# Performance work log

Hardware: AMD Instinct MI355X
Metric: run time of the kernel (lower is better)

## Reference

```python
import jax, jax.numpy as jnp
import numpy as np
from jax import lax

T, A, F = 32, 32, 4          # tokens, analyses per token, feats per analysis
E = 256; FE = F * E          # feat emb dim, flattened analysis emb (1024)
H = 768; H2 = 2 * H          # encoder hidden (bi), decoder hidden 1536
DTOK = 256; DDEC = FE + DTOK # decoder input: analysis emb + token emb
V = 50000; VTOK = 30000


def setup_inputs() -> dict:
    key = jax.random.key(0)
    ks = jax.random.split(key, 16)
    g = lambda k, sh, s=0.02: (jax.random.normal(k, sh, jnp.float32) * s)
    return {
        "lattice": jax.random.randint(ks[0], (1, T, A, F), 0, V),
        "lattice_mask": jnp.ones((1, T, A), bool),
        "inputs": jax.random.randint(ks[1], (1, T), 0, VTOK),
        "input_lengths": jnp.full((1, 1, 1), T, jnp.int32),
        "gold_indices": jax.random.randint(ks[2], (1, T), 0, A),
        "sos_ids": jax.random.randint(ks[3], (F,), 0, V),
        "emb_table": g(ks[4], (V, E), 0.1),
        "tok_emb_table": g(ks[5], (VTOK, DTOK), 0.1),
        "enc_Wx_f": g(ks[6], (FE, 4 * H)),
        "enc_Wh_f": g(ks[7], (H, 4 * H)),
        "enc_b_f": jnp.zeros(4 * H, jnp.float32),
        "enc_Wx_b": g(ks[8], (FE, 4 * H)),
        "enc_Wh_b": g(ks[9], (H, 4 * H)),
        "enc_b_b": jnp.zeros(4 * H, jnp.float32),
        "dec_Wx": g(ks[10], (DDEC, 4 * H2)),
        "dec_Wh": g(ks[11], (H2, 4 * H2)),
        "dec_b": jnp.zeros(4 * H2, jnp.float32),
        "attn_W": g(ks[12], (H2, H2)),
    }


def _lstm(xs, Wx, Wh, b, hsize, reverse=False):
    # torch LSTM gate order: i, f, g, o
    def step(carry, x):
        h, c = carry
        gt = x @ Wx + h @ Wh + b
        i, f, g, o = jnp.split(gt, 4)
        c = jax.nn.sigmoid(f) * c + jax.nn.sigmoid(i) * jnp.tanh(g)
        h = jax.nn.sigmoid(o) * jnp.tanh(c)
        return (h, c), h
    init = (jnp.zeros(hsize, xs.dtype), jnp.zeros(hsize, xs.dtype))
    (h, c), ys = lax.scan(step, init, xs, reverse=reverse)
    return ys, h, c


def reference(lattice, lattice_mask, inputs, input_lengths, gold_indices, sos_ids,
              emb_table, tok_emb_table,
              enc_Wx_f, enc_Wh_f, enc_b_f, enc_Wx_b, enc_Wh_b, enc_b_b,
              dec_Wx, dec_Wh, dec_b, attn_W):
    # lattice_emb: per-feat embedding, flattened per analysis -> [1,T,A,FE]
    embed_lattice = emb_table[lattice].reshape(1, T, A, FE)
    # mask is all-True, so mask-packing == flatten: [T*A, FE]
    packed = embed_lattice.reshape(T * A, FE)
    ys_f, hf, cf = _lstm(packed, enc_Wx_f, enc_Wh_f, enc_b_f, H)
    ys_b, hb, cb = _lstm(packed, enc_Wx_b, enc_Wh_b, enc_b_b, H, reverse=True)
    enc = jnp.concatenate([ys_f, ys_b], axis=-1).reshape(T, A, H2)  # per-token slices
    h0 = jnp.concatenate([hf, hb])  # decoder init = concat(fwd,bwd) final states
    c0 = jnp.concatenate([cf, cb])
    tok_emb = tok_emb_table[inputs[0]]          # [T, DTOK]
    sos_emb = emb_table[sos_ids].reshape(FE)    # SOS analysis embedding
    lat = embed_lattice[0]                      # [T, A, FE]

    def step(carry, xs_t):
        h, c, prev = carry
        enc_t, tok_t, g_t, lat_t = xs_t
        x = jnp.concatenate([prev, tok_t])      # [DDEC]
        gt = x @ dec_Wx + h @ dec_Wh + dec_b
        i, f, g, o = jnp.split(gt, 4)
        c_n = jax.nn.sigmoid(f) * c + jax.nn.sigmoid(i) * jnp.tanh(g)
        h_n = jax.nn.sigmoid(o) * jnp.tanh(c_n)
        score = (h_n @ attn_W) @ enc_t.T        # bilinear attention scores [A]
        # teacher forcing: next analysis emb gathered by gold index
        return (h_n, c_n, lat_t[g_t]), score

    _, scores = lax.scan(step, (h0, c0, sos_emb), (enc, tok_emb, gold_indices[0], lat))
    return scores[None]  # [1, T, A]
```

## Files before the change

### kernel.cpp

```cpp
#include <hip/hip_runtime.h>
#include <cstddef>
#include <cstdint>

#define T_ 32
#define A_ 32
#define F_ 4
#define E_ 256
#define FE_ 1024
#define H_ 768
#define H2_ 1536
#define G4_ 3072
#define G8_ 6144
#define DTOK_ 256
#define DDEC_ 1280
#define SEQ_ 1024

constexpr size_t OFF_PACKED  = 0;
constexpr size_t OFF_XF      = OFF_PACKED + 1024ull*1024;
constexpr size_t OFF_XB      = OFF_XF + 1024ull*3072;
constexpr size_t OFF_XD      = OFF_XB + 1024ull*3072;
constexpr size_t OFF_XDIN    = OFF_XD + 32*6144;
constexpr size_t OFF_ENC     = OFF_XDIN + 32*1280;
constexpr size_t OFF_HN      = OFF_ENC + 1024ull*1536;
constexpr size_t OFF_AMAT    = OFF_HN + 32*1536;
constexpr size_t OFF_C0      = OFF_AMAT + 32*1536;
constexpr size_t OFF_PAIRS_E = OFF_C0 + 1536;
constexpr size_t OFF_PAIRS_D = OFF_PAIRS_E + 6144;
constexpr size_t MEMSET_BYTES = (6144 + 6144) * 4;

__device__ __forceinline__ float sigf(float x) { return 1.f / (1.f + __expf(-x)); }

__global__ void embed_k(const int* __restrict__ lattice, const int* __restrict__ inputs,
                        const int* __restrict__ gold, const int* __restrict__ sos,
                        const float* __restrict__ emb, const float* __restrict__ tok_emb,
                        float* __restrict__ packed, float* __restrict__ xdec_in) {
    int b = blockIdx.x, tid = threadIdx.x;
    if (b < SEQ_) {
        #pragma unroll
        for (int f = 0; f < F_; ++f) {
            int vid = lattice[b * F_ + f];
            packed[(size_t)b * FE_ + f * E_ + tid] = emb[(size_t)vid * E_ + tid];
        }
    } else {
        int t = b - SEQ_;
        for (int j = tid; j < DDEC_; j += 256) {
            float v;
            if (j < FE_) {
                int f = j >> 8, e2 = j & 255;
                int vid = (t == 0) ? sos[f]
                                   : lattice[(((t - 1) * A_) + gold[t - 1]) * F_ + f];
                v = emb[(size_t)vid * E_ + e2];
            } else {
                v = tok_emb[(size_t)inputs[t] * DTOK_ + (j - FE_)];
            }
            xdec_in[(size_t)t * DDEC_ + j] = v;
        }
    }
}

#define BM 128
#define BN 128
#define BK 8
__device__ __forceinline__ void gemm_body(
    const float* __restrict__ A, const float* __restrict__ B,
    const float* __restrict__ bias, float* __restrict__ C,
    int M, int N, int K, int n0, int m0, int swh) {
    __shared__ float As[BK][BM + 4];
    __shared__ float Bs[BK][BN + 4];
    int tid = threadIdx.x;
    int tx = tid & 15, ty = tid >> 4;
    int lam = tid >> 1, lak = (tid & 1) * 4;
    int lbk = tid >> 5, lbn = (tid & 31) * 4;
    float acc[8][8] = {};
    for (int k0 = 0; k0 < K; k0 += BK) {
        float4 av = make_float4(0.f, 0.f, 0.f, 0.f);
        if (m0 + lam < M)
            av = *(const float4*)(A + (size_t)(m0 + lam) * K + k0 + lak);
        float4 bv = *(const float4*)(B + (size_t)(k0 + lbk) * N + n0 + lbn);
        __syncthreads();
        As[lak + 0][lam] = av.x; As[lak + 1][lam] = av.y;
        As[lak + 2][lam] = av.z; As[lak + 3][lam] = av.w;
        *(float4*)&Bs[lbk][lbn] = bv;
        __syncthreads();
        #pragma unroll
        for (int kk = 0; kk < BK; ++kk) {
            float a[8], b[8];
            *(float4*)&a[0] = *(const float4*)&As[kk][ty * 8];
            *(float4*)&a[4] = *(const float4*)&As[kk][ty * 8 + 4];
            *(float4*)&b[0] = *(const float4*)&Bs[kk][tx * 8];
            *(float4*)&b[4] = *(const float4*)&Bs[kk][tx * 8 + 4];
            #pragma unroll
            for (int i = 0; i < 8; ++i)
                #pragma unroll
                for (int j = 0; j < 8; ++j)
                    acc[i][j] += a[i] * b[j];
        }
    }
    int qg = 0, jb = 0;
    if (swh) { qg = n0 / swh; jb = n0 - qg * swh; }
    #pragma unroll
    for (int i = 0; i < 8; ++i) {
        int m = m0 + ty * 8 + i;
        if (m >= M) break;
        #pragma unroll
        for (int j = 0; j < 8; ++j) {
            int n = n0 + tx * 8 + j;
            float bb = bias ? bias[n] : 0.f;
            float v = acc[i][j] + bb;
            if (swh) {
                int jc = jb + tx * 8 + j;
                n = (jc / 12) * 48 + (jc % 12) * 4 + qg;
            }
            C[(size_t)m * N + n] = v;
        }
    }
}

__global__ __launch_bounds__(256) void gemm_bias_k(
    const float* __restrict__ A, const float* __restrict__ B,
    const float* __restrict__ bias, float* __restrict__ C,
    int M, int N, int K, int swh) {
    gemm_body(A, B, bias, C, M, N, K, blockIdx.x * BN, blockIdx.y * BM, swh);
}

__global__ __launch_bounds__(256) void gemm_bias2_k(
    const float* __restrict__ A,
    const float* __restrict__ B0, const float* __restrict__ bias0, float* __restrict__ C0,
    const float* __restrict__ B1, const float* __restrict__ bias1, float* __restrict__ C1,
    int M, int N, int K, int swh) {
    const float* B = blockIdx.z ? B1 : B0;
    const float* bias = blockIdx.z ? bias1 : bias0;
    float* C = blockIdx.z ? C1 : C0;
    gemm_body(A, B, bias, C, M, N, K, blockIdx.x * BN, blockIdx.y * BM, swh);
}

__global__ __launch_bounds__(768, 1) void lstm_enc_k(
    const float* __restrict__ Xf, const float* __restrict__ Xb,
    const float* __restrict__ Whf, const float* __restrict__ Whb,
    float* __restrict__ enc, unsigned long long* __restrict__ pairsE,
    unsigned long long* __restrict__ pairsD, float* __restrict__ c0) {
    const int dir = blockIdx.x >> 6;
    const int wb  = blockIdx.x & 63;
    const float* X  = dir ? Xb : Xf;
    const float* Wh = dir ? Whb : Whf;
    unsigned long long* pp = pairsE + (size_t)dir * 1536;
    const int tid = threadIdx.x;
    const int w = tid >> 6, lane = tid & 63;
    const int g16 = lane >> 4;
    const int jg = wb * 12 + w;
    const int d = lane >> 2, q = lane & 3;

    float wgt[3][4][4];
    #pragma unroll
    for (int i = 0; i < 3; ++i)
        #pragma unroll
        for (int e = 0; e < 4; ++e) {
            int k = 4 * lane + e + 256 * i;
            #pragma unroll
            for (int g = 0; g < 4; ++g)
                wgt[i][e][g] = Wh[(size_t)k * G4_ + g * H_ + jg];
        }
    #pragma unroll
    for (int i = 0; i < 3; ++i)
        #pragma unroll
        for (int e = 0; e < 4; ++e)
            #pragma unroll
            for (int g = 0; g < 4; ++g)
                asm volatile("" : "+v"(wgt[i][e][g]));

    __shared__ float h_s[2][768];
    __shared__ float part[4][64];
    float c = 0.f;

    for (int t = 0; t < SEQ_; ++t) {
        const int row = dir ? (SEQ_ - 1 - t) : t;
        float xq = 0.f;
        if (w == 0 && lane < 48) xq = X[(size_t)row * G4_ + wb * 48 + lane];

        const int par = t & 1;
        unsigned long long* p = pp + par * 768 + tid;
        unsigned long long v = __hip_atomic_load(p, __ATOMIC_RELAXED, __HIP_MEMORY_SCOPE_AGENT);
        while ((unsigned)(v >> 32) != (unsigned)t)
            v = __hip_atomic_load(p, __ATOMIC_RELAXED, __HIP_MEMORY_SCOPE_AGENT);
        h_s[par][tid] = __uint_as_float((unsigned)v);
        __syncthreads();

        float a0 = 0.f, a1 = 0.f, a2 = 0.f, a3 = 0.f;
        #pragma unroll
        for (int i = 0; i < 3; ++i) {
            const float4 hv = *(const float4*)&h_s[par][4 * lane + 256 * i];
            a0 += wgt[i][0][0] * hv.x + wgt[i][1][0] * hv.y + wgt[i][2][0] * hv.z + wgt[i][3][0] * hv.w;
            a1 += wgt[i][0][1] * hv.x + wgt[i][1][1] * hv.y + wgt[i][2][1] * hv.z + wgt[i][3][1] * hv.w;
            a2 += wgt[i][0][2] * hv.x + wgt[i][1][2] * hv.y + wgt[i][2][2] * hv.z + wgt[i][3][2] * hv.w;
            a3 += wgt[i][0][3] * hv.x + wgt[i][1][3] * hv.y + wgt[i][2][3] * hv.z + wgt[i][3][3] * hv.w;
        }
        #pragma unroll
        for (int m = 1; m < 16; m <<= 1) {
            a0 += __shfl_xor(a0, m); a1 += __shfl_xor(a1, m);
            a2 += __shfl_xor(a2, m); a3 += __shfl_xor(a3, m);
        }
        if ((lane & 15) == 0)
            *(float4*)&part[g16][w * 4] = make_float4(a0, a1, a2, a3);
        __syncthreads();

        if (w == 0) {
            float s = part[0][lane] + part[1][lane] + part[2][lane] + part[3][lane] + xq;
            float tr = (q == 2) ? tanhf(s) : sigf(s);
            float b1 = __shfl_xor(tr, 1), b2 = __shfl_xor(tr, 2), b3 = __shfl_xor(tr, 3);
            float I  = (q == 0) ? tr : (q == 1) ? b1 : (q == 2) ? b2 : b3;
            float Fv = (q == 0) ? b1 : (q == 1) ? tr : (q == 2) ? b3 : b2;
            float G  = (q == 0) ? b2 : (q == 1) ? b3 : (q == 2) ? tr : b1;
            float O  = (q == 0) ? b3 : (q == 1) ? b2 : (q == 2) ? b1 : tr;
            c = Fv * c + I * G;
            float h = O * tanhf(c);
            float hc = __shfl(h, lane * 4);
            if (lane < 12) {
                enc[(size_t)row * H2_ + dir * H_ + wb * 12 + lane] = hc;
                unsigned long long pk = ((unsigned long long)(unsigned)(t + 1) << 32)
                                      | (unsigned long long)__float_as_uint(hc);
                __hip_atomic_store(pp + ((t + 1) & 1) * 768 + wb * 12 + lane, pk,
                                   __ATOMIC_RELAXED, __HIP_MEMORY_SCOPE_AGENT);
            }
            if (t == SEQ_ - 1) {
                float cc = __shfl(c, lane * 4);
                if (lane < 12) {
                    __hip_atomic_store(pairsD + (size_t)(dir * H_ + wb * 12 + lane),
                                       (unsigned long long)__float_as_uint(hc),
                                       __ATOMIC_RELAXED, __HIP_MEMORY_SCOPE_AGENT);
                    c0[dir * H_ + wb * 12 + lane] = cc;
                }
            }
        }
    }
}

__global__ __launch_bounds__(768, 1) void lstm_dec_k(
    const float* __restrict__ Xd, const float* __restrict__ Wh,
    float* __restrict__ Hn, unsigned long long* __restrict__ pairs,
    const float* __restrict__ c0) {
    const int wb = blockIdx.x;
    const int tid = threadIdx.x;
    const int w = tid >> 6, lane = tid & 63;
    const int g16 = lane >> 4;
    const int jg = wb * 12 + w;
    const int d = lane >> 2, q = lane & 3;

    float wgt[6][4][4];
    #pragma unroll
    for (int i = 0; i < 6; ++i)
        #pragma unroll
        for (int e = 0; e < 4; ++e) {
            int k = 4 * lane + e + 256 * i;
            #pragma unroll
            for (int g = 0; g < 4; ++g)
                wgt[i][e][g] = Wh[(size_t)k * G8_ + g * H2_ + jg];
        }
    #pragma unroll
    for (int i = 0; i < 6; ++i)
        #pragma unroll
        for (int e = 0; e < 4; ++e)
            #pragma unroll
            for (int g = 0; g < 4; ++g)
                asm volatile("" : "+v"(wgt[i][e][g]));

    __shared__ float h_s[2][1536];
    __shared__ float part[4][64];
    float c = (w == 0 && lane < 48) ? c0[wb * 12 + d] : 0.f;

    for (int t = 0; t < T_; ++t) {
        float xq = 0.f;
        if (w == 0 && lane < 48) xq = Xd[(size_t)t * G8_ + wb * 48 + lane];

        const int par = t & 1;
        unsigned long long* p0 = pairs + par * 1536 + tid;
        unsigned long long* p1 = p0 + 768;
        unsigned long long v0 = __hip_atomic_load(p0, __ATOMIC_RELAXED, __HIP_MEMORY_SCOPE_AGENT);
        unsigned long long v1 = __hip_atomic_load(p1, __ATOMIC_RELAXED, __HIP_MEMORY_SCOPE_AGENT);
        while ((unsigned)(v0 >> 32) != (unsigned)t)
            v0 = __hip_atomic_load(p0, __ATOMIC_RELAXED, __HIP_MEMORY_SCOPE_AGENT);
        while ((unsigned)(v1 >> 32) != (unsigned)t)
            v1 = __hip_atomic_load(p1, __ATOMIC_RELAXED, __HIP_MEMORY_SCOPE_AGENT);
        h_s[par][tid]       = __uint_as_float((unsigned)v0);
        h_s[par][tid + 768] = __uint_as_float((unsigned)v1);
        __syncthreads();

        float a0 = 0.f, a1 = 0.f, a2 = 0.f, a3 = 0.f;
        #pragma unroll
        for (int i = 0; i < 6; ++i) {
            const float4 hv = *(const float4*)&h_s[par][4 * lane + 256 * i];
            a0 += wgt[i][0][0] * hv.x + wgt[i][1][0] * hv.y + wgt[i][2][0] * hv.z + wgt[i][3][0] * hv.w;
            a1 += wgt[i][0][1] * hv.x + wgt[i][1][1] * hv.y + wgt[i][2][1] * hv.z + wgt[i][3][1] * hv.w;
            a2 += wgt[i][0][2] * hv.x + wgt[i][1][2] * hv.y + wgt[i][2][2] * hv.z + wgt[i][3][2] * hv.w;
            a3 += wgt[i][0][3] * hv.x + wgt[i][1][3] * hv.y + wgt[i][2][3] * hv.z + wgt[i][3][3] * hv.w;
        }
        #pragma unroll
        for (int m = 1; m < 16; m <<= 1) {
            a0 += __shfl_xor(a0, m); a1 += __shfl_xor(a1, m);
            a2 += __shfl_xor(a2, m); a3 += __shfl_xor(a3, m);
        }
        if ((lane & 15) == 0)
            *(float4*)&part[g16][w * 4] = make_float4(a0, a1, a2, a3);
        __syncthreads();

        if (w == 0) {
            float s = part[0][lane] + part[1][lane] + part[2][lane] + part[3][lane] + xq;
            float tr = (q == 2) ? tanhf(s) : sigf(s);
            float b1 = __shfl_xor(tr, 1), b2 = __shfl_xor(tr, 2), b3 = __shfl_xor(tr, 3);
            float I  = (q == 0) ? tr : (q == 1) ? b1 : (q == 2) ? b2 : b3;
            float Fv = (q == 0) ? b1 : (q == 1) ? tr : (q == 2) ? b3 : b2;
            float G  = (q == 0) ? b2 : (q == 1) ? b3 : (q == 2) ? tr : b1;
            float O  = (q == 0) ? b3 : (q == 1) ? b2 : (q == 2) ? b1 : tr;
            c = Fv * c + I * G;
            float h = O * tanhf(c);
            float hc = __shfl(h, lane * 4);
            if (lane < 12) {
                Hn[(size_t)t * H2_ + wb * 12 + lane] = hc;
                unsigned long long pk = ((unsigned long long)(unsigned)(t + 1) << 32)
                                      | (unsigned long long)__float_as_uint(hc);
                __hip_atomic_store(pairs + ((t + 1) & 1) * 1536 + wb * 12 + lane, pk,
                                   __ATOMIC_RELAXED, __HIP_MEMORY_SCOPE_AGENT);
            }
        }
    }
}

__global__ void score_k(const float* __restrict__ Amat, const float* __restrict__ enc,
                        float* __restrict__ outp) {
    int t = blockIdx.x, tid = threadIdx.x;
    __shared__ float a_s[H2_];
    for (int i = tid; i < H2_; i += 256) a_s[i] = Amat[(size_t)t * H2_ + i];
    __syncthreads();
    int aa = tid >> 3, p = tid & 7;
    const float4* e = (const float4*)(enc + (size_t)(t * A_ + aa) * H2_ + p * 192);
    const float4* ap = (const float4*)(a_s + p * 192);
    float s = 0.f;
    #pragma unroll
    for (int i = 0; i < 48; ++i) {
        float4 av = ap[i], ev = e[i];
        s += av.x * ev.x + av.y * ev.y + av.z * ev.z + av.w * ev.w;
    }
    s += __shfl_xor(s, 1); s += __shfl_xor(s, 2); s += __shfl_xor(s, 4);
    if (p == 0) outp[t * A_ + aa] = s;
}

extern "C" void kernel_launch(void* const* d_in, const int* in_sizes, int n_in,
                              void* d_out, int out_size, void* d_ws, size_t ws_size,
                              hipStream_t stream) {
    const int*   lattice = (const int*)d_in[0];
    const int*   inputs  = (const int*)d_in[2];
    const int*   gold    = (const int*)d_in[4];
    const int*   sos     = (const int*)d_in[5];
    const float* emb     = (const float*)d_in[6];
    const float* tok     = (const float*)d_in[7];
    const float* Wxf = (const float*)d_in[8];
    const float* Whf = (const float*)d_in[9];
    const float* bf  = (const float*)d_in[10];
    const float* Wxb = (const float*)d_in[11];
    const float* Whb = (const float*)d_in[12];
    const float* bb  = (const float*)d_in[13];
    const float* dWx = (const float*)d_in[14];
    const float* dWh = (const float*)d_in[15];
    const float* db  = (const float*)d_in[16];
    const float* aW  = (const float*)d_in[17];
    float* ws  = (float*)d_ws;
    float* out = (float*)d_out;

    float* packed = ws + OFF_PACKED;
    float* Xf     = ws + OFF_XF;
    float* Xb     = ws + OFF_XB;
    float* Xd     = ws + OFF_XD;
    float* xdin   = ws + OFF_XDIN;
    float* enc    = ws + OFF_ENC;
    float* Hn     = ws + OFF_HN;
    float* Amat   = ws + OFF_AMAT;
    float* c0     = ws + OFF_C0;
    unsigned long long* pairsE = (unsigned long long*)(ws + OFF_PAIRS_E);
    unsigned long long* pairsD = (unsigned long long*)(ws + OFF_PAIRS_D);

    hipMemsetAsync((char*)d_ws + OFF_PAIRS_E * sizeof(float), 0, MEMSET_BYTES, stream);

    embed_k<<<SEQ_ + T_, 256, 0, stream>>>(lattice, inputs, gold, sos, emb, tok,
                                           packed, xdin);
    gemm_bias2_k<<<dim3(G4_ / BN, SEQ_ / BM, 2), 256, 0, stream>>>(
        packed, Wxf, bf, Xf, Wxb, bb, Xb, SEQ_, G4_, FE_, H_);
    gemm_bias_k<<<dim3(G8_ / BN, 1), 256, 0, stream>>>(xdin, dWx, db, Xd,
                                                       T_, G8_, DDEC_, H2_);
    lstm_enc_k<<<128, 768, 0, stream>>>(Xf, Xb, Whf, Whb, enc, pairsE, pairsD, c0);
    lstm_dec_k<<<128, 768, 0, stream>>>(Xd, dWh, Hn, pairsD, c0);
    gemm_bias_k<<<dim3(H2_ / BN, 1), 256, 0, stream>>>(Hn, aW, nullptr, Amat,
                                                       T_, H2_, H2_, 0);
    score_k<<<T_, 256, 0, stream>>>(Amat, enc, out);
}
```

Measured before the change: 3.224 ms.

## Halve encoder LSTM block count with two hidden units per warp, add spin sleep

The encoder recurrent kernel now runs 32 blocks per direction instead of 64. Each warp keeps weights for two hidden units in registers, so each block covers 24 units. The goal is fewer blocks taking part in the per-step global atomic handshake, with fewer flag loads and less contention. In exchange each block does twice the arithmetic per step and holds twice the register-resident weights, which risks spilling. The gate-input GEMM's output interleave is made configurable to match the new grouping, and s_sleep is added to the spin-wait loops in both recurrent kernels to cut polling pressure, at the cost of some wake-up latency.

```diff
diff --git a/kernel.cpp b/kernel.cpp
--- a/kernel.cpp
+++ b/kernel.cpp
@@ -64,7 +64,7 @@
 __device__ __forceinline__ void gemm_body(
     const float* __restrict__ A, const float* __restrict__ B,
     const float* __restrict__ bias, float* __restrict__ C,
-    int M, int N, int K, int n0, int m0, int swh) {
+    int M, int N, int K, int n0, int m0, int swh, int dbs) {
     __shared__ float As[BK][BM + 4];
     __shared__ float Bs[BK][BN + 4];
     int tid = threadIdx.x;
@@ -109,7 +109,7 @@
             float v = acc[i][j] + bb;
             if (swh) {
                 int jc = jb + tx * 8 + j;
-                n = (jc / 12) * 48 + (jc % 12) * 4 + qg;
+                n = (jc / dbs) * (4 * dbs) + (jc % dbs) * 4 + qg;
             }
             C[(size_t)m * N + n] = v;
         }
@@ -119,19 +119,19 @@
 __global__ __launch_bounds__(256) void gemm_bias_k(
     const float* __restrict__ A, const float* __restrict__ B,
     const float* __restrict__ bias, float* __restrict__ C,
-    int M, int N, int K, int swh) {
-    gemm_body(A, B, bias, C, M, N, K, blockIdx.x * BN, blockIdx.y * BM, swh);
+    int M, int N, int K, int swh, int dbs) {
+    gemm_body(A, B, bias, C, M, N, K, blockIdx.x * BN, blockIdx.y * BM, swh, dbs);
 }
 
 __global__ __launch_bounds__(256) void gemm_bias2_k(
     const float* __restrict__ A,
     const float* __restrict__ B0, const float* __restrict__ bias0, float* __restrict__ C0,
     const float* __restrict__ B1, const float* __restrict__ bias1, float* __restrict__ C1,
-    int M, int N, int K, int swh) {
+    int M, int N, int K, int swh, int dbs) {
     const float* B = blockIdx.z ? B1 : B0;
     const float* bias = blockIdx.z ? bias1 : bias0;
     float* C = blockIdx.z ? C1 : C0;
-    gemm_body(A, B, bias, C, M, N, K, blockIdx.x * BN, blockIdx.y * BM, swh);
+    gemm_body(A, B, bias, C, M, N, K, blockIdx.x * BN, blockIdx.y * BM, swh, dbs);
 }
 
 __global__ __launch_bounds__(768, 1) void lstm_enc_k(
@@ -139,95 +139,112 @@
     const float* __restrict__ Whf, const float* __restrict__ Whb,
     float* __restrict__ enc, unsigned long long* __restrict__ pairsE,
     unsigned long long* __restrict__ pairsD, float* __restrict__ c0) {
-    const int dir = blockIdx.x >> 6;
-    const int wb  = blockIdx.x & 63;
+    const int dir = blockIdx.x >> 5;
+    const int wb  = blockIdx.x & 31;
     const float* X  = dir ? Xb : Xf;
     const float* Wh = dir ? Whb : Whf;
     unsigned long long* pp = pairsE + (size_t)dir * 1536;
     const int tid = threadIdx.x;
-    const int w = tid >> 6, lane = tid & 63;
-    const int g16 = lane >> 4;
-    const int jg = wb * 12 + w;
-    const int d = lane >> 2, q = lane & 3;
-
-    float wgt[3][4][4];
-    #pragma unroll
-    for (int i = 0; i < 3; ++i)
-        #pragma unroll
-        for (int e = 0; e < 4; ++e) {
-            int k = 4 * lane + e + 256 * i;
+    const int w = tid >> 6, lane = tid & 63, g16 = lane >> 4;
+
+    float wgt[2][3][4][4];
+    #pragma unroll
+    for (int l = 0; l < 2; ++l)
+        #pragma unroll
+        for (int i = 0; i < 3; ++i)
             #pragma unroll
-            for (int g = 0; g < 4; ++g)
-                wgt[i][e][g] = Wh[(size_t)k * G4_ + g * H_ + jg];
-        }
-    #pragma unroll
-    for (int i = 0; i < 3; ++i)
-        #pragma unroll
-        for (int e = 0; e < 4; ++e)
+            for (int e = 0; e < 4; ++e) {
+                int k = 4 * lane + e + 256 * i;
+                #pragma unroll
+                for (int g = 0; g < 4; ++g)
+                    wgt[l][i][e][g] = Wh[(size_t)k * G4_ + g * H_ + wb * 24 + 2 * w + l];
+            }
+    #pragma unroll
+    for (int l = 0; l < 2; ++l)
+        #pragma unroll
+        for (int i = 0; i < 3; ++i)
             #pragma unroll
-            for (int g = 0; g < 4; ++g)
-                asm volatile("" : "+v"(wgt[i][e][g]));
+            for (int e = 0; e < 4; ++e)
+                #pragma unroll
+                for (int g = 0; g < 4; ++g)
+                    asm volatile("" : "+v"(wgt[l][i][e][g]));
 
     __shared__ float h_s[2][768];
-    __shared__ float part[4][64];
+    __shared__ float part[4][104];
     float c = 0.f;
 
     for (int t = 0; t < SEQ_; ++t) {
         const int row = dir ? (SEQ_ - 1 - t) : t;
         float xq = 0.f;
-        if (w == 0 && lane < 48) xq = X[(size_t)row * G4_ + wb * 48 + lane];
+        if (w < 2 && lane < 48)
+            xq = X[(size_t)row * G4_ + wb * 96 + w * 48 + lane];
 
         const int par = t & 1;
         unsigned long long* p = pp + par * 768 + tid;
         unsigned long long v = __hip_atomic_load(p, __ATOMIC_RELAXED, __HIP_MEMORY_SCOPE_AGENT);
-        while ((unsigned)(v >> 32) != (unsigned)t)
+        while ((unsigned)(v >> 32) != (unsigned)t) {
+            __builtin_amdgcn_s_sleep(1);
             v = __hip_atomic_load(p, __ATOMIC_RELAXED, __HIP_MEMORY_SCOPE_AGENT);
+        }
         h_s[par][tid] = __uint_as_float((unsigned)v);
         __syncthreads();
 
         float a0 = 0.f, a1 = 0.f, a2 = 0.f, a3 = 0.f;
+        float b0 = 0.f, b1 = 0.f, b2 = 0.f, b3 = 0.f;
         #pragma unroll
         for (int i = 0; i < 3; ++i) {
             const float4 hv = *(const float4*)&h_s[par][4 * lane + 256 * i];
-            a0 += wgt[i][0][0] * hv.x + wgt[i][1][0] * hv.y + wgt[i][2][0] * hv.z + wgt[i][3][0] * hv.w;
-            a1 += wgt[i][0][1] * hv.x + wgt[i][1][1] * hv.y + wgt[i][2][1] * hv.z + wgt[i][3][1] * hv.w;
-            a2 += wgt[i][0][2] * hv.x + wgt[i][1][2] * hv.y + wgt[i][2][2] * hv.z + wgt[i][3][2] * hv.w;
-            a3 += wgt[i][0][3] * hv.x + wgt[i][1][3] * hv.y + wgt[i][2][3] * hv.z + wgt[i][3][3] * hv.w;
+            a0 += wgt[0][i][0][0] * hv.x + wgt[0][i][1][0] * hv.y + wgt[0][i][2][0] * hv.z + wgt[0][i][3][0] * hv.w;
+            a1 += wgt[0][i][0][1] * hv.x + wgt[0][i][1][1] * hv.y + wgt[0][i][2][1] * hv.z + wgt[0][i][3][1] * hv.w;
+            a2 += wgt[0][i][0][2] * hv.x + wgt[0][i][1][2] * hv.y + wgt[0][i][2][2] * hv.z + wgt[0][i][3][2] * hv.w;
+            a3 += wgt[0][i][0][3] * hv.x + wgt[0][i][1][3] * hv.y + wgt[0][i][2][3] * hv.z + wgt[0][i][3][3] * hv.w;
+            b0 += wgt[1][i][0][0] * hv.x + wgt[1][i][1][0] * hv.y + wgt[1][i][2][0] * hv.z + wgt[1][i][3][0] * hv.w;
+            b1 += wgt[1][i][0][1] * hv.x + wgt[1][i][1][1] * hv.y + wgt[1][i][2][1] * hv.z + wgt[1][i][3][1] * hv.w;
+            b2 += wgt[1][i][0][2] * hv.x + wgt[1][i][1][2] * hv.y + wgt[1][i][2][2] * hv.z + wgt[1][i][3][2] * hv.w;
+            b3 += wgt[1][i][0][3] * hv.x + wgt[1][i][1][3] * hv.y + wgt[1][i][2][3] * hv.z + wgt[1][i][3][3] * hv.w;
         }
         #pragma unroll
         for (int m = 1; m < 16; m <<= 1) {
             a0 += __shfl_xor(a0, m); a1 += __shfl_xor(a1, m);
             a2 += __shfl_xor(a2, m); a3 += __shfl_xor(a3, m);
-        }
-        if ((lane & 15) == 0)
-            *(float4*)&part[g16][w * 4] = make_float4(a0, a1, a2, a3);
-        __syncthreads();
-
-        if (w == 0) {
-            float s = part[0][lane] + part[1][lane] + part[2][lane] + part[3][lane] + xq;
+            b0 += __shfl_xor(b0, m); b1 += __shfl_xor(b1, m);
+            b2 += __shfl_xor(b2, m); b3 += __shfl_xor(b3, m);
+        }
+        if ((lane & 15) == 0) {
+            *(float4*)&part[g16][w * 8]     = make_float4(a0, a1, a2, a3);
+            *(float4*)&part[g16][w * 8 + 4] = make_float4(b0, b1, b2, b3);
+        }
+        __syncthreads();
+
+        if (w < 2 && lane < 48) {
+            const int dd = w * 12 + (lane >> 2), q = lane & 3;
+            const int po = (dd >> 1) * 8 + (dd & 1) * 4 + q;
+            float s = part[0][po] + part[1][po] + part[2][po] + part[3][po] + xq;
             float tr = (q == 2) ? tanhf(s) : sigf(s);
-            float b1 = __shfl_xor(tr, 1), b2 = __shfl_xor(tr, 2), b3 = __shfl_xor(tr, 3);
-            float I  = (q == 0) ? tr : (q == 1) ? b1 : (q == 2) ? b2 : b3;
-            float Fv = (q == 0) ? b1 : (q == 1) ? tr : (q == 2) ? b3 : b2;
-            float G  = (q == 0) ? b2 : (q == 1) ? b3 : (q == 2) ? tr : b1;
-            float O  = (q == 0) ? b3 : (q == 1) ? b2 : (q == 2) ? b1 : tr;
+            float s1 = __shfl_xor(tr, 1), s2 = __shfl_xor(tr, 2), s3 = __shfl_xor(tr, 3);
+            float I  = (q == 0) ? tr : (q == 1) ? s1 : (q == 2) ? s2 : s3;
+            float Fv = (q == 0) ? s1 : (q == 1) ? tr : (q == 2) ? s3 : s2;
+            float G  = (q == 0) ? s2 : (q == 1) ? s3 : (q == 2) ? tr : s1;
+            float O  = (q == 0) ? s3 : (q == 1) ? s2 : (q == 2) ? s1 : tr;
             c = Fv * c + I * G;
             float h = O * tanhf(c);
             float hc = __shfl(h, lane * 4);
             if (lane < 12) {
-                enc[(size_t)row * H2_ + dir * H_ + wb * 12 + lane] = hc;
+                const int idx = wb * 24 + w * 12 + lane;
+                enc[(size_t)row * H2_ + dir * H_ + idx] = hc;
                 unsigned long long pk = ((unsigned long long)(unsigned)(t + 1) << 32)
                                       | (unsigned long long)__float_as_uint(hc);
-                __hip_atomic_store(pp + ((t + 1) & 1) * 768 + wb * 12 + lane, pk,
+                __hip_atomic_store(pp + ((t + 1) & 1) * 768 + idx, pk,
                                    __ATOMIC_RELAXED, __HIP_MEMORY_SCOPE_AGENT);
             }
             if (t == SEQ_ - 1) {
                 float cc = __shfl(c, lane * 4);
                 if (lane < 12) {
-                    __hip_atomic_store(pairsD + (size_t)(dir * H_ + wb * 12 + lane),
+                    const int idx = wb * 24 + w * 12 + lane;
+                    __hip_atomic_store(pairsD + (size_t)(dir * H_ + idx),
                                        (unsigned long long)__float_as_uint(hc),
                                        __ATOMIC_RELAXED, __HIP_MEMORY_SCOPE_AGENT);
-                    c0[dir * H_ + wb * 12 + lane] = cc;
+                    c0[dir * H_ + idx] = cc;
                 }
             }
         }
@@ -275,11 +292,15 @@
         unsigned long long* p0 = pairs + par * 1536 + tid;
         unsigned long long* p1 = p0 + 768;
         unsigned long long v0 = __hip_atomic_load(p0, __ATOMIC_RELAXED, __HIP_MEMORY_SCOPE_AGENT);
+        while ((unsigned)(v0 >> 32) != (unsigned)t) {
+            __builtin_amdgcn_s_sleep(1);
+            v0 = __hip_atomic_load(p0, __ATOMIC_RELAXED, __HIP_MEMORY_SCOPE_AGENT);
+        }
         unsigned long long v1 = __hip_atomic_load(p1, __ATOMIC_RELAXED, __HIP_MEMORY_SCOPE_AGENT);
-        while ((unsigned)(v0 >> 32) != (unsigned)t)
-            v0 = __hip_atomic_load(p0, __ATOMIC_RELAXED, __HIP_MEMORY_SCOPE_AGENT);
-        while ((unsigned)(v1 >> 32) != (unsigned)t)
+        while ((unsigned)(v1 >> 32) != (unsigned)t) {
+            __builtin_amdgcn_s_sleep(1);
             v1 = __hip_atomic_load(p1, __ATOMIC_RELAXED, __HIP_MEMORY_SCOPE_AGENT);
+        }
         h_s[par][tid]       = __uint_as_float((unsigned)v0);
         h_s[par][tid + 768] = __uint_as_float((unsigned)v1);
         __syncthreads();
@@ -305,11 +326,11 @@
         if (w == 0) {
             float s = part[0][lane] + part[1][lane] + part[2][lane] + part[3][lane] + xq;
             float tr = (q == 2) ? tanhf(s) : sigf(s);
-            float b1 = __shfl_xor(tr, 1), b2 = __shfl_xor(tr, 2), b3 = __shfl_xor(tr, 3);
-            float I  = (q == 0) ? tr : (q == 1) ? b1 : (q == 2) ? b2 : b3;
-            float Fv = (q == 0) ? b1 : (q == 1) ? tr : (q == 2) ? b3 : b2;
-            float G  = (q == 0) ? b2 : (q == 1) ? b3 : (q == 2) ? tr : b1;
-            float O  = (q == 0) ? b3 : (q == 1) ? b2 : (q == 2) ? b1 : tr;
+            float s1 = __shfl_xor(tr, 1), s2 = __shfl_xor(tr, 2), s3 = __shfl_xor(tr, 3);
+            float I  = (q == 0) ? tr : (q == 1) ? s1 : (q == 2) ? s2 : s3;
+            float Fv = (q == 0) ? s1 : (q == 1) ? tr : (q == 2) ? s3 : s2;
+            float G  = (q == 0) ? s2 : (q == 1) ? s3 : (q == 2) ? tr : s1;
+            float O  = (q == 0) ? s3 : (q == 1) ? s2 : (q == 2) ? s1 : tr;
             c = Fv * c + I * G;
             float h = O * tanhf(c);
             float hc = __shfl(h, lane * 4);
@@ -382,12 +403,12 @@
     embed_k<<<SEQ_ + T_, 256, 0, stream>>>(lattice, inputs, gold, sos, emb, tok,
                                            packed, xdin);
     gemm_bias2_k<<<dim3(G4_ / BN, SEQ_ / BM, 2), 256, 0, stream>>>(
-        packed, Wxf, bf, Xf, Wxb, bb, Xb, SEQ_, G4_, FE_, H_);
+        packed, Wxf, bf, Xf, Wxb, bb, Xb, SEQ_, G4_, FE_, H_, 24);
     gemm_bias_k<<<dim3(G8_ / BN, 1), 256, 0, stream>>>(xdin, dWx, db, Xd,
-                                                       T_, G8_, DDEC_, H2_);
-    lstm_enc_k<<<128, 768, 0, stream>>>(Xf, Xb, Whf, Whb, enc, pairsE, pairsD, c0);
+                                                       T_, G8_, DDEC_, H2_, 12);
+    lstm_enc_k<<<64, 768, 0, stream>>>(Xf, Xb, Whf, Whb, enc, pairsE, pairsD, c0);
     lstm_dec_k<<<128, 768, 0, stream>>>(Xd, dWh, Hn, pairsD, c0);
     gemm_bias_k<<<dim3(H2_ / BN, 1), 256, 0, stream>>>(Hn, aW, nullptr, Amat,
-                                                       T_, H2_, H2_, 0);
+                                                       T_, H2_, H2_, 0, 1);
     score_k<<<T_, 256, 0, stream>>>(Amat, enc, out);
 }
```

New measurement: 3.694 ms. 1.15x slower.
